# Optimization experiments

Hardware: AMD Instinct MI355X
Metric: run time of the kernel (lower is better)

## Reference

```python
import jax, jax.numpy as jnp
import numpy as np

RES = (64, 64)
TEMP = 0.1  # forward default temp

def _mgrid(res):
    # matches torch.meshgrid(linspace(0, r-1, r)...) with default 'ij' indexing
    gs = jnp.meshgrid(*[jnp.arange(r, dtype=jnp.float32) for r in res], indexing='ij')
    return jnp.stack(gs, 0)  # [2, H, W]

def setup_inputs() -> dict:
    key = jax.random.key(0)
    k1, k2 = jax.random.split(key)
    x = jax.random.normal(k1, (8, 32, RES[0], RES[1]), dtype=jnp.float32)
    of = jax.random.normal(k2, (8, 2, RES[0], RES[1]), dtype=jnp.float32)
    return {"x": x, "of": of}

def reference(x, of):
    bs, C = x.shape[0], x.shape[1]
    hw = RES[0] * RES[1]
    gpos = _mgrid(RES).reshape(2, hw)                 # [2, HW] target pixel positions
    opos = gpos[None] + of.reshape(bs, 2, hw)         # [bs, 2, HW] flow-displaced source positions
    # L1 distance: logits[b, i, j] = sum_c |opos[b, c, j] - gpos[c, i]|
    dist = jnp.abs(opos[:, :, None, :] - gpos[None, :, :, None]).sum(axis=1)  # [bs, HW, HW]
    # softmax over target axis i (dim=-2 in torch) -> each source pixel j distributes mass over targets
    locs = jax.nn.softmax(-dist / TEMP, axis=1)       # [bs, HW, HW]
    # out[b, c, i] = sum_j x[b, c, j] * locs[b, i, j]
    out = jnp.einsum('bij,bcj->bci', locs, x.reshape(bs, C, hw))
    return out.reshape(bs, C, RES[0], RES[1])
```

## Files before the change

kernel.cpp:

```cpp
#include <hip/hip_runtime.h>
#include <math.h>

#define HW    4096
#define NC    32
#define NB    8
#define TINV  10.0f
#define RWIN  8
#define WDIM  (8 + 2 * RWIN)
#define RCUT  2.5f


__global__ __launch_bounds__(256) void prep_kernel(
    const float* __restrict__ x, const float* __restrict__ of,
    float4* __restrict__ params, float* __restrict__ xt)
{
    __shared__ float tile[32][257];
    int b  = blockIdx.x >> 4;
    int j0 = (blockIdx.x & 15) << 8;
    int t  = threadIdx.x;
    int j  = j0 + t;

    float oy = (float)(j >> 6) + of[(b * 2 + 0) * HW + j];
    float ox = (float)(j & 63) + of[(b * 2 + 1) * HW + j];

    int cy0 = min(max((int)floorf(oy), 0), 63);
    int cx0 = min(max((int)floorf(ox), 0), 63);
    float Dy = 0.f, Dx = 0.f;
    #pragma unroll
    for (int d = -3; d <= 3; ++d) {
        int iy = cy0 + d, ix = cx0 + d;
        if ((unsigned)iy < 64u) Dy += __expf(-TINV * fabsf(oy - (float)iy));
        if ((unsigned)ix < 64u) Dx += __expf(-TINV * fabsf(ox - (float)ix));
    }
    params[(b << 12) + j] = make_float4(oy, ox, 1.f / Dy, 1.f / Dx);

    #pragma unroll
    for (int c = 0; c < NC; ++c)
        tile[c][t] = x[((b * NC + c) << 12) + j];
    __syncthreads();
    #pragma unroll
    for (int k = 0; k < NC; ++k) {
        int o  = k * 256 + t;
        int jj = o >> 5, c = o & 31;
        xt[((size_t)((b << 12) + j0 + jj)) * NC + c] = tile[c][jj];
    }
}

__global__ __launch_bounds__(256) void gather_kernel(
    const float4* __restrict__ params, const float4* __restrict__ xt4,
    float* __restrict__ out)
{
    __shared__ float4 wp[4][64];
    __shared__ int    sj[4][64];
    __shared__ float  pool[4 * 64 * 17];

    const int b    = blockIdx.z;
    const int h    = blockIdx.y;
    const int tile = blockIdx.x;
    const int ty0  = (tile >> 3) << 3;
    const int tx0  = (tile & 7) << 3;

    const int tid  = threadIdx.x;
    const int lane = tid & 63;
    const int wv   = __builtin_amdgcn_readfirstlane(tid >> 6);

    const float iy = (float)(ty0 + (lane >> 3));
    const float ix = (float)(tx0 + (lane & 7));

    float acc[16];
    #pragma unroll
    for (int c = 0; c < 16; ++c) acc[c] = 0.f;

    const float4* pb = params + (b << 12);
    const float4* xb = xt4 + (size_t)(b << 12) * 8 + h * 4;

    const int srow = lane >> 5;
    const int scol = lane & 31;
    const int sidq = lane >> 2;
    const int quad = lane & 3;

    float* XS = pool;

    for (int r = 0; r < 3; ++r) {
        int ry = wv + srow * 4 + r * 8;
        int jy = ty0 - RWIN + ry;
        int jx = tx0 - RWIN + scol;
        bool valid = ((unsigned)jy < 64u) && ((unsigned)jx < 64u) && (scol < WDIM);
        int j = (jy << 6) + jx;
        float4 p = pb[valid ? j : 0];
        float cy = fminf(fmaxf(p.x, 0.f), 63.f);
        float cx = fminf(fmaxf(p.y, 0.f), 63.f);
        float dyr = fmaxf(fmaxf((float)ty0 - cy, cy - ((float)ty0 + 7.f)), 0.f);
        float dxr = fmaxf(fmaxf((float)tx0 - cx, cx - ((float)tx0 + 7.f)), 0.f);
        bool pred = valid && (dyr + dxr < RCUT);

        unsigned long long m = __ballot(pred);
        int cnt = __popcll(m);
        if (pred) {
            int pos = __builtin_amdgcn_mbcnt_hi((unsigned)(m >> 32),
                      __builtin_amdgcn_mbcnt_lo((unsigned)m, 0u));
            wp[wv][pos] = p;
            sj[wv][pos] = j;
        }

        for (int m4 = 0; m4 < cnt; m4 += 16) {
            int s = sidq + m4;
            if (s < cnt) {
                int jj = sj[wv][s];
                float4 v = xb[jj * 8 + quad];
                *(float4*)&XS[((wv << 6) + s) * 16 + (quad << 2)] = v;
            }
        }

        for (int k = 0; k < cnt; k += 2) {
            int i1 = min(k + 1, cnt - 1);
            float4 p0 = wp[wv][k], p1 = wp[wv][i1];
            const float* x0 = &XS[((wv << 6) + k)  * 16];
            const float* x1 = &XS[((wv << 6) + i1) * 16];
            float4 A[4], B[4];
            #pragma unroll
            for (int u = 0; u < 4; ++u) A[u] = ((const float4*)x0)[u];
            #pragma unroll
            for (int u = 0; u < 4; ++u) B[u] = ((const float4*)x1)[u];

            float g0 = (__expf(-TINV * fabsf(p0.x - iy)) * p0.z)
                     * (__expf(-TINV * fabsf(p0.y - ix)) * p0.w);
            float g1 = (__expf(-TINV * fabsf(p1.x - iy)) * p1.z)
                     * (__expf(-TINV * fabsf(p1.y - ix)) * p1.w);
            g1 = (k + 1 < cnt) ? g1 : 0.f;

            #pragma unroll
            for (int u = 0; u < 4; ++u) {
                acc[4*u+0] = fmaf(g0, A[u].x, acc[4*u+0]);
                acc[4*u+1] = fmaf(g0, A[u].y, acc[4*u+1]);
                acc[4*u+2] = fmaf(g0, A[u].z, acc[4*u+2]);
                acc[4*u+3] = fmaf(g0, A[u].w, acc[4*u+3]);
            }
            #pragma unroll
            for (int u = 0; u < 4; ++u) {
                acc[4*u+0] = fmaf(g1, B[u].x, acc[4*u+0]);
                acc[4*u+1] = fmaf(g1, B[u].y, acc[4*u+1]);
                acc[4*u+2] = fmaf(g1, B[u].z, acc[4*u+2]);
                acc[4*u+3] = fmaf(g1, B[u].w, acc[4*u+3]);
            }
        }
    }

    __syncthreads();
    float* red = pool;
    float* myred = red + ((wv << 6) + lane) * 17;
    #pragma unroll
    for (int c = 0; c < 16; ++c) myred[c] = acc[c];
    __syncthreads();

    int c   = tid >> 4;
    int t16 = tid & 15;
    #pragma unroll
    for (int k = 0; k < 4; ++k) {
        int t = t16 + 16 * k;
        float s = red[(0 * 64 + t) * 17 + c]
                + red[(1 * 64 + t) * 17 + c]
                + red[(2 * 64 + t) * 17 + c]
                + red[(3 * 64 + t) * 17 + c];
        int ch = h * 16 + c;
        out[(((b << 5) + ch) << 12) + (ty0 + (t >> 3)) * 64 + (tx0 + (t & 7))] = s;
    }
}

extern "C" void kernel_launch(void* const* d_in, const int* in_sizes, int n_in,
                              void* d_out, int out_size, void* d_ws, size_t ws_size,
                              hipStream_t stream) {
    const float* x  = (const float*)d_in[0];
    const float* of = (const float*)d_in[1];
    float* out = (float*)d_out;

    float4* params = (float4*)d_ws;
    float*  xt     = (float*)((char*)d_ws + NB * HW * sizeof(float4));

    prep_kernel<<<dim3(NB * 16), dim3(256), 0, stream>>>(x, of, params, xt);
    gather_kernel<<<dim3(64, 2, NB), dim3(256), 0, stream>>>(params, (const float4*)xt, out);
}
```

Baseline: 72.41 us.

## Use bf16 MFMA for the windowed gather-weighted channel accumulation

New measurement: 73.30 us. No clear change (+1.2%).

```diff
diff --git a/kernel.cpp b/kernel.cpp
--- a/kernel.cpp
+++ b/kernel.cpp
@@ -8,6 +8,14 @@
 #define RWIN  8
 #define WDIM  (8 + 2 * RWIN)
 #define RCUT  2.5f
+
+typedef __attribute__((ext_vector_type(8))) short short8;
+typedef __attribute__((ext_vector_type(4))) float f32x4;
+
+__device__ __forceinline__ unsigned short bf16rtn(float f) {
+    unsigned int u = __float_as_uint(f);
+    return (unsigned short)((u + 0x7FFFu + ((u >> 16) & 1u)) >> 16);
+}
 
 
 __global__ __launch_bounds__(256) void prep_kernel(
@@ -50,9 +58,10 @@
     const float4* __restrict__ params, const float4* __restrict__ xt4,
     float* __restrict__ out)
 {
-    __shared__ float4 wp[4][64];
-    __shared__ int    sj[4][64];
-    __shared__ float  pool[4 * 64 * 17];
+    __shared__ float          wpf[4][64 * 5];
+    __shared__ int            sjl[4][64];
+    __shared__ unsigned short XS[4][16][66];
+    __shared__ float          red[4 * 64 * 17];
 
     const int b    = blockIdx.z;
     const int h    = blockIdx.y;
@@ -64,22 +73,19 @@
     const int lane = tid & 63;
     const int wv   = __builtin_amdgcn_readfirstlane(tid >> 6);
 
-    const float iy = (float)(ty0 + (lane >> 3));
-    const float ix = (float)(tx0 + (lane & 7));
-
-    float acc[16];
-    #pragma unroll
-    for (int c = 0; c < 16; ++c) acc[c] = 0.f;
+    const int   L   = lane & 15;
+    const float ixl = (float)(tx0 + (L & 7));
+    const float iy0 = (float)(ty0 + (L >> 3));
+
+    f32x4 acc[4];
+    #pragma unroll
+    for (int mt = 0; mt < 4; ++mt) acc[mt] = (f32x4){0.f, 0.f, 0.f, 0.f};
 
     const float4* pb = params + (b << 12);
     const float4* xb = xt4 + (size_t)(b << 12) * 8 + h * 4;
 
     const int srow = lane >> 5;
     const int scol = lane & 31;
-    const int sidq = lane >> 2;
-    const int quad = lane & 3;
-
-    float* XS = pool;
 
     for (int r = 0; r < 3; ++r) {
         int ry = wv + srow * 4 + r * 8;
@@ -99,58 +105,74 @@
         if (pred) {
             int pos = __builtin_amdgcn_mbcnt_hi((unsigned)(m >> 32),
                       __builtin_amdgcn_mbcnt_lo((unsigned)m, 0u));
-            wp[wv][pos] = p;
-            sj[wv][pos] = j;
-        }
-
-        for (int m4 = 0; m4 < cnt; m4 += 16) {
-            int s = sidq + m4;
+            float* wq = &wpf[wv][pos * 5];
+            wq[0] = p.x; wq[1] = p.y; wq[2] = p.z; wq[3] = p.w;
+            sjl[wv][pos] = j;
+        }
+        if (cnt == 0) continue;
+
+        unsigned int* xz = (unsigned int*)&XS[wv][0][0];
+        #pragma unroll
+        for (int i = 0; i < 9; ++i) {
+            int idx = lane + (i << 6);
+            if (idx < 528) xz[idx] = 0u;
+        }
+
+        for (int base = 0; base < cnt; base += 16) {
+            int s = base + (lane >> 2);
             if (s < cnt) {
-                int jj = sj[wv][s];
-                float4 v = xb[jj * 8 + quad];
-                *(float4*)&XS[((wv << 6) + s) * 16 + (quad << 2)] = v;
+                int jj = sjl[wv][s];
+                float4 v = xb[jj * 8 + (lane & 3)];
+                int c0 = (lane & 3) << 2;
+                XS[wv][c0 + 0][s] = bf16rtn(v.x);
+                XS[wv][c0 + 1][s] = bf16rtn(v.y);
+                XS[wv][c0 + 2][s] = bf16rtn(v.z);
+                XS[wv][c0 + 3][s] = bf16rtn(v.w);
             }
         }
 
-        for (int k = 0; k < cnt; k += 2) {
-            int i1 = min(k + 1, cnt - 1);
-            float4 p0 = wp[wv][k], p1 = wp[wv][i1];
-            const float* x0 = &XS[((wv << 6) + k)  * 16];
-            const float* x1 = &XS[((wv << 6) + i1) * 16];
-            float4 A[4], B[4];
+        int ksteps = (cnt + 31) >> 5;
+        int kchunk = (lane >> 4) << 3;
+        for (int ks = 0; ks < ksteps; ++ks) {
+            int kbase = (ks << 5) + kchunk;
+
+            short8 av[4];
             #pragma unroll
-            for (int u = 0; u < 4; ++u) A[u] = ((const float4*)x0)[u];
+            for (int jj8 = 0; jj8 < 8; ++jj8) {
+                int k  = kbase + jj8;
+                int kc = min(k, cnt - 1);
+                const float* pp = &wpf[wv][kc * 5];
+                float wx = __expf(-TINV * fabsf(pp[1] - ixl)) * pp[3];
+                bool real = (k < cnt);
+                #pragma unroll
+                for (int mt = 0; mt < 4; ++mt) {
+                    float wy = __expf(-TINV * fabsf(pp[0] - (iy0 + 2.f * mt)))
+                             * pp[2];
+                    float w  = wy * wx;
+                    av[mt][jj8] = real ? (short)bf16rtn(w) : (short)0;
+                }
+            }
+
+            union { unsigned int u[4]; short8 v; } bu;
+            const unsigned int* xr = (const unsigned int*)&XS[wv][L][kbase];
+            bu.u[0] = xr[0]; bu.u[1] = xr[1]; bu.u[2] = xr[2]; bu.u[3] = xr[3];
+
             #pragma unroll
-            for (int u = 0; u < 4; ++u) B[u] = ((const float4*)x1)[u];
-
-            float g0 = (__expf(-TINV * fabsf(p0.x - iy)) * p0.z)
-                     * (__expf(-TINV * fabsf(p0.y - ix)) * p0.w);
-            float g1 = (__expf(-TINV * fabsf(p1.x - iy)) * p1.z)
-                     * (__expf(-TINV * fabsf(p1.y - ix)) * p1.w);
-            g1 = (k + 1 < cnt) ? g1 : 0.f;
-
-            #pragma unroll
-            for (int u = 0; u < 4; ++u) {
-                acc[4*u+0] = fmaf(g0, A[u].x, acc[4*u+0]);
-                acc[4*u+1] = fmaf(g0, A[u].y, acc[4*u+1]);
-                acc[4*u+2] = fmaf(g0, A[u].z, acc[4*u+2]);
-                acc[4*u+3] = fmaf(g0, A[u].w, acc[4*u+3]);
-            }
-            #pragma unroll
-            for (int u = 0; u < 4; ++u) {
-                acc[4*u+0] = fmaf(g1, B[u].x, acc[4*u+0]);
-                acc[4*u+1] = fmaf(g1, B[u].y, acc[4*u+1]);
-                acc[4*u+2] = fmaf(g1, B[u].z, acc[4*u+2]);
-                acc[4*u+3] = fmaf(g1, B[u].w, acc[4*u+3]);
-            }
+            for (int mt = 0; mt < 4; ++mt)
+                acc[mt] = __builtin_amdgcn_mfma_f32_16x16x32_bf16(
+                              av[mt], bu.v, acc[mt], 0, 0, 0);
         }
     }
 
     __syncthreads();
-    float* red = pool;
-    float* myred = red + ((wv << 6) + lane) * 17;
-    #pragma unroll
-    for (int c = 0; c < 16; ++c) myred[c] = acc[c];
+    #pragma unroll
+    for (int mt = 0; mt < 4; ++mt) {
+        #pragma unroll
+        for (int rr = 0; rr < 4; ++rr) {
+            int t = (mt << 4) + ((lane >> 4) << 2) + rr;
+            red[((wv << 6) + t) * 17 + L] = acc[mt][rr];
+        }
+    }
     __syncthreads();
 
     int c   = tid >> 4;
```
